# Kernel tuning notes

Hardware: AMD Instinct MI355X
Metric: run time of the kernel (lower is better)

## Reference

```python
import jax, jax.numpy as jnp
import numpy as np

MAX_LOGIT = 30.0
COV_WEIGHT = 1.0


def setup_inputs() -> dict:
    key = jax.random.key(0)
    ks = jax.random.split(key, 8)
    B, T, S, H = 8, 100, 400, 256
    sc = 1.0 / np.sqrt(H)
    return {
        "decoder_outputs": jax.random.normal(ks[0], (B, T, H), jnp.float32),
        "encoder_outputs": jax.random.normal(ks[1], (B, S, H), jnp.float32),
        "src_mask": jnp.zeros((B, S), dtype=bool),
        "W_h": jax.random.normal(ks[2], (H, H), jnp.float32) * sc,
        "W_s": jax.random.normal(ks[3], (H, H), jnp.float32) * sc,
        "w_c": jax.random.normal(ks[4], (H,), jnp.float32) * sc,  # Linear(1,H) weight
        "v": jax.random.normal(ks[5], (H,), jnp.float32) * sc,    # Linear(H,1) weight
        "b_attn": jnp.zeros((H,), jnp.float32),
    }


def reference(decoder_outputs, encoder_outputs, src_mask, W_h, W_s, w_c, v, b_attn):
    B, T, H = decoder_outputs.shape
    S = encoder_outputs.shape[1]
    neg_inf = jnp.float32(-jnp.inf)

    Wh = jnp.einsum('bsh,hk->bsk', encoder_outputs, W_h)   # [B,S,H]
    Ws = jnp.einsum('bth,hk->btk', decoder_outputs, W_s)   # [B,T,H]
    # E_base: [B,T,S,H]
    E_base = Wh[:, None, :, :] + Ws[:, :, None, :] + b_attn

    def logits(x):
        e = jnp.einsum('btsh,h->bts', jnp.tanh(x), v)
        e = jnp.clip(e, -MAX_LOGIT, MAX_LOGIT)
        return jnp.where(src_mask[:, None, :], neg_inf, e)

    A_prelim = jax.nn.softmax(logits(E_base), axis=-1)      # [B,T,S]
    cum = jnp.cumsum(A_prelim, axis=1)
    cov_shifted = jnp.concatenate(
        [jnp.zeros((B, 1, S), A_prelim.dtype), cum[:, :-1, :]], axis=1)  # [B,T,S]

    # W_c applied to scalar coverage: outer product with w_c -> [B,T,S,H]
    E_final = logits(E_base + cov_shifted[..., None] * w_c)
    A_final = jax.nn.softmax(E_final, axis=-1)              # [B,T,S]

    context = jnp.einsum('bts,bsh->bth', A_final, encoder_outputs)
    cov_loss = (COV_WEIGHT * jnp.sum(jnp.minimum(A_final, cov_shifted), axis=-1).mean())[None]
    return context, A_final, cov_loss
```

## Files before the change

kernel.cpp:

```cpp
#include <hip/hip_runtime.h>
#include <math.h>

#define B_ 8
#define T_ 100
#define S_ 400
#define H_ 256
#define HQ_ (H_ / 4)
#define BT_ (B_ * T_)
#define MAXL 30.0f
#define K_EXP 2.885390081777927f

#define AF_OFF (BT_ * H_)
#define LOSS_OFF (BT_ * H_ + BT_ * S_)

#define EWHT_OFF 0
#define EWSB_OFF (B_ * H_ * S_)
#define ACOV_OFF (EWSB_OFF + BT_ * H_)

#define EC1 0.6931471806f
#define EC2 0.2402265070f
#define EC3 0.0555041087f
#define EC4 0.0096181291f

__device__ __forceinline__ float wave_sum(float p) {
#pragma unroll
    for (int off = 32; off; off >>= 1) p += __shfl_xor(p, off, 64);
    return p;
}

__device__ __forceinline__ float wave_max(float p) {
#pragma unroll
    for (int off = 32; off; off >>= 1) p = fmaxf(p, __shfl_xor(p, off, 64));
    return p;
}

#define ROWS 8
__global__ __launch_bounds__(256) void k_gemm(
    const float* __restrict__ dec, const float* __restrict__ enc,
    const float* __restrict__ W_h, const float* __restrict__ W_s,
    const float* __restrict__ b_attn,
    float* __restrict__ EWhT4, float* __restrict__ EWsb) {
    const int tid = threadIdx.x;
    const int blk = blockIdx.x;
    const int NB_ENC = (B_ * S_) / ROWS;

    float acc[ROWS];
#pragma unroll
    for (int r = 0; r < ROWS; ++r) acc[r] = 0.f;

    if (blk < NB_ENC) {
        const int r0 = blk * ROWS;
        const int b = r0 / S_, s0 = r0 - b * S_;
        const float* in = enc + (size_t)r0 * H_;
        const float* Wp = W_h + tid;
#pragma unroll 4
        for (int h = 0; h < H_; ++h) {
            float w = Wp[(size_t)h * H_];
#pragma unroll
            for (int r = 0; r < ROWS; ++r)
                acc[r] = fmaf(in[r * H_ + h], w, acc[r]);
        }
        float* o = EWhT4 + (((size_t)b * HQ_ + (tid >> 2)) * S_ + s0) * 4 + (tid & 3);
#pragma unroll
        for (int r = 0; r < ROWS; ++r)
            o[r * 4] = __builtin_amdgcn_exp2f(K_EXP * acc[r]);
    } else {
        const int bt0 = (blk - NB_ENC) * ROWS;
        const float* in = dec + (size_t)bt0 * H_;
        const float* Wp = W_s + tid;
        const float bias = b_attn[tid];
#pragma unroll 4
        for (int h = 0; h < H_; ++h) {
            float w = Wp[(size_t)h * H_];
#pragma unroll
            for (int r = 0; r < ROWS; ++r)
                acc[r] = fmaf(in[r * H_ + h], w, acc[r]);
        }
#pragma unroll
        for (int r = 0; r < ROWS; ++r)
            EWsb[(size_t)(bt0 + r) * H_ + tid] =
                __builtin_amdgcn_exp2f(K_EXP * (acc[r] + bias));
    }
}

__global__ __launch_bounds__(1024) void k_prelim(
    const float* __restrict__ EWhT4, const float* __restrict__ EWsb,
    const float* __restrict__ v,
    const unsigned char* __restrict__ mask,
    float* __restrict__ A) {
    __shared__ float red[32];
    const int blk = blockIdx.x;
    const int b = blk & 7;
    const int tp = blk >> 3;
    const int tid = threadIdx.x;
    const int hh = tid >> 9;
    const int s = tid & 511;
    const int bt = b * T_ + 2 * tp + hh;
    const int lane = tid & 63;
    const int wid = tid >> 6;
    const bool act = (s < S_);

    const float4 vv4 = *reinterpret_cast<const float4*>(v + 4 * lane);
    const float sumv = wave_sum((vv4.x + vv4.y) + (vv4.z + vv4.w));

    const float* E = EWsb + (size_t)bt * H_;
    float acc = 0.f;
    if (act) {
        const float4* eq = reinterpret_cast<const float4*>(
                               EWhT4 + (size_t)b * HQ_ * S_ * 4) + s;
#pragma unroll 4
        for (int hq = 0; hq < HQ_; ++hq) {
            const float4 Ew = eq[(size_t)hq * S_];
            const int h = 4 * hq;
            const float v0 = v[h], v1 = v[h + 1], v2 = v[h + 2], v3 = v[h + 3];
            float p0 = fmaf(Ew.x, E[h], 1.f);
            float p1 = fmaf(Ew.y, E[h + 1], 1.f);
            float p2 = fmaf(Ew.z, E[h + 2], 1.f);
            float p3 = fmaf(Ew.w, E[h + 3], 1.f);
            float p01 = p0 * p1, p23 = p2 * p3;
            float num = fmaf(fmaf(v0, p1, v1 * p0), p23,
                             fmaf(v2, p3, v3 * p2) * p01);
            acc = fmaf(num, __builtin_amdgcn_rcpf(p01 * p23), acc);
        }
    }

    float e = -INFINITY;
    if (act) {
        e = fminf(fmaxf(sumv - 2.f * acc, -MAXL), MAXL);
        if (mask[(size_t)b * S_ + s]) e = -INFINITY;
    }

    float mx = wave_max(e);
    if (lane == 0) red[wid] = mx;
    __syncthreads();
    {
        const float* r8 = red + 8 * hh;
        mx = fmaxf(fmaxf(fmaxf(r8[0], r8[1]), fmaxf(r8[2], r8[3])),
                   fmaxf(fmaxf(r8[4], r8[5]), fmaxf(r8[6], r8[7])));
    }

    float p = act ? __expf(e - mx) : 0.f;
    float sm = wave_sum(p);
    if (lane == 0) red[16 + wid] = sm;
    __syncthreads();
    {
        const float* r8 = red + 16 + 8 * hh;
        sm = ((r8[0] + r8[1]) + (r8[2] + r8[3])) +
             ((r8[4] + r8[5]) + (r8[6] + r8[7]));
    }

    if (act) A[(size_t)bt * S_ + s] = p * __builtin_amdgcn_rcpf(sm);
}

__global__ __launch_bounds__(64) void k_cumsum(float* __restrict__ A,
                                               float* __restrict__ out) {
    const int idx = blockIdx.x * 64 + threadIdx.x;
    if (idx == 0) out[LOSS_OFF] = 0.f;
    if (idx >= B_ * S_) return;
    const int b = idx / S_;
    const int s = idx - b * S_;
    float* col = A + (size_t)b * T_ * S_ + s;
    float run = 0.f;
#pragma unroll 10
    for (int t = 0; t < T_; ++t) {
        float a = col[(size_t)t * S_];
        col[(size_t)t * S_] = run;
        run += a;
    }
}

__global__ __launch_bounds__(1024) void k_final(
    const float* __restrict__ EWhT4, const float* __restrict__ EWsb,
    const float* __restrict__ v, const float* __restrict__ w_c,
    const float* __restrict__ cov,
    const unsigned char* __restrict__ mask,
    const float* __restrict__ enc,
    float* __restrict__ out) {
    __shared__ float e_lds[2][512];
    __shared__ float ctxp[2 * H_];
    __shared__ float red[32];
    const int blk = blockIdx.x;
    const int b = blk & 7;
    const int tp = blk >> 3;
    const int bt0 = b * T_ + 2 * tp;
    const int tid = threadIdx.x;
    const int hh = tid >> 9;
    const int s = tid & 511;
    const int bt = bt0 + hh;
    const int lane = tid & 63;
    const int wid = tid >> 6;
    const bool act = (s < S_);

    const float4 vv4 = *reinterpret_cast<const float4*>(v + 4 * lane);
    const float sumv = wave_sum((vv4.x + vv4.y) + (vv4.z + vv4.w));

    float c = 0.f;
    if (act) c = cov[(size_t)bt * S_ + s];
    const float ck = K_EXP * c;

    const float* E = EWsb + (size_t)bt * H_;
    float acc = 0.f;
    if (act) {
        const float4* eq = reinterpret_cast<const float4*>(
                               EWhT4 + (size_t)b * HQ_ * S_ * 4) + s;
#pragma unroll 2
        for (int hq = 0; hq < HQ_; ++hq) {
            const float4 Ew = eq[(size_t)hq * S_];
            const int h = 4 * hq;
            const float v0 = v[h], v1 = v[h + 1], v2 = v[h + 2], v3 = v[h + 3];
            float x0 = ck * w_c[h];
            float x1 = ck * w_c[h + 1];
            float x2 = ck * w_c[h + 2];
            float x3 = ck * w_c[h + 3];
            float Ec0 = fmaf(x0, fmaf(x0, fmaf(x0, fmaf(x0, EC4, EC3), EC2), EC1), 1.f);
            float Ec1 = fmaf(x1, fmaf(x1, fmaf(x1, fmaf(x1, EC4, EC3), EC2), EC1), 1.f);
            float Ec2 = fmaf(x2, fmaf(x2, fmaf(x2, fmaf(x2, EC4, EC3), EC2), EC1), 1.f);
            float Ec3 = fmaf(x3, fmaf(x3, fmaf(x3, fmaf(x3, EC4, EC3), EC2), EC1), 1.f);
            float p0 = fmaf(Ew.x * E[h], Ec0, 1.f);
            float p1 = fmaf(Ew.y * E[h + 1], Ec1, 1.f);
            float p2 = fmaf(Ew.z * E[h + 2], Ec2, 1.f);
            float p3 = fmaf(Ew.w * E[h + 3], Ec3, 1.f);
            float p01 = p0 * p1, p23 = p2 * p3;
            float num = fmaf(fmaf(v0, p1, v1 * p0), p23,
                             fmaf(v2, p3, v3 * p2) * p01);
            acc = fmaf(num, __builtin_amdgcn_rcpf(p01 * p23), acc);
        }
    }

    float e = -INFINITY;
    if (act) {
        e = fminf(fmaxf(sumv - 2.f * acc, -MAXL), MAXL);
        if (mask[(size_t)b * S_ + s]) e = -INFINITY;
    }

    float mx = wave_max(e);
    if (lane == 0) red[wid] = mx;
    __syncthreads();
    {
        const float* r8 = red + 8 * hh;
        mx = fmaxf(fmaxf(fmaxf(r8[0], r8[1]), fmaxf(r8[2], r8[3])),
                   fmaxf(fmaxf(r8[4], r8[5]), fmaxf(r8[6], r8[7])));
    }

    float p = act ? __expf(e - mx) : 0.f;
    float sm = wave_sum(p);
    if (lane == 0) red[16 + wid] = sm;
    __syncthreads();
    {
        const float* r8 = red + 16 + 8 * hh;
        sm = ((r8[0] + r8[1]) + (r8[2] + r8[3])) +
             ((r8[4] + r8[5]) + (r8[6] + r8[7]));
    }

    const float a = act ? p * __builtin_amdgcn_rcpf(sm) : 0.f;

    float lp = act ? fminf(a, c) : 0.f;
    lp = wave_sum(lp);
    if (lane == 0) red[wid] = lp;

    if (act) {
        e_lds[hh][s] = a;
        out[AF_OFF + (size_t)bt * S_ + s] = a;
    }
    __syncthreads();

    if (tid == 0) {
        float tot = 0.f;
#pragma unroll
        for (int i = 0; i < 16; ++i) tot += red[i];
        atomicAdd(out + LOSS_OFF, tot * (1.0f / (B_ * T_)));
    }

    const int q = tid >> 8;
    const int h = tid & (H_ - 1);
    const int ts = q & 1;
    const int sb = (q >> 1) * (S_ / 2);
    const float* el = e_lds[ts];
    const float* eb = enc + ((size_t)b * S_ + sb) * H_ + h;
    float q0 = 0.f, q1 = 0.f, q2 = 0.f, q3 = 0.f;
#pragma unroll 5
    for (int j = 0; j < S_ / 2; j += 4) {
        q0 = fmaf(el[sb + j], eb[(size_t)j * H_], q0);
        q1 = fmaf(el[sb + j + 1], eb[(size_t)(j + 1) * H_], q1);
        q2 = fmaf(el[sb + j + 2], eb[(size_t)(j + 2) * H_], q2);
        q3 = fmaf(el[sb + j + 3], eb[(size_t)(j + 3) * H_], q3);
    }
    const float r = (q0 + q1) + (q2 + q3);
    if ((q >> 1) == 0) ctxp[ts * H_ + h] = r;
    __syncthreads();
    if ((q >> 1) == 1)
        out[(size_t)(bt0 + ts) * H_ + h] = ctxp[ts * H_ + h] + r;
}

extern "C" void kernel_launch(void* const* d_in, const int* in_sizes, int n_in,
                              void* d_out, int out_size, void* d_ws, size_t ws_size,
                              hipStream_t stream) {
    const float* dec = (const float*)d_in[0];
    const float* enc = (const float*)d_in[1];
    const unsigned char* mask = (const unsigned char*)d_in[2];
    const float* W_h = (const float*)d_in[3];
    const float* W_s = (const float*)d_in[4];
    const float* w_c = (const float*)d_in[5];
    const float* v = (const float*)d_in[6];
    const float* b_attn = (const float*)d_in[7];

    float* out = (float*)d_out;
    float* ws = (float*)d_ws;
    float* EWhT4 = ws + EWHT_OFF;
    float* EWsb = ws + EWSB_OFF;
    float* Acov = ws + ACOV_OFF;

    const int nb_gemm = (B_ * S_) / ROWS + BT_ / ROWS;
    const int nb_pair = B_ * (T_ / 2);
    k_gemm<<<nb_gemm, 256, 0, stream>>>(dec, enc, W_h, W_s, b_attn, EWhT4, EWsb);
    k_prelim<<<nb_pair, 1024, 0, stream>>>(EWhT4, EWsb, v, mask, Acov);
    k_cumsum<<<(B_ * S_ + 63) / 64, 64, 0, stream>>>(Acov, out);
    k_final<<<nb_pair, 1024, 0, stream>>>(EWhT4, EWsb, v, w_c, Acov, mask, enc, out);
}
```

Measured before the change: 177.2 us.

## Split H across half-blocks so each Ew load serves two decoder rows

```diff
diff --git a/kernel.cpp b/kernel.cpp
--- a/kernel.cpp
+++ b/kernel.cpp
@@ -16,11 +16,6 @@
 #define EWHT_OFF 0
 #define EWSB_OFF (B_ * H_ * S_)
 #define ACOV_OFF (EWSB_OFF + BT_ * H_)
-
-#define EC1 0.6931471806f
-#define EC2 0.2402265070f
-#define EC3 0.0555041087f
-#define EC4 0.0096181291f
 
 __device__ __forceinline__ float wave_sum(float p) {
 #pragma unroll
@@ -88,14 +83,15 @@
     const float* __restrict__ v,
     const unsigned char* __restrict__ mask,
     float* __restrict__ A) {
+    __shared__ float part[2][512][2];
     __shared__ float red[32];
     const int blk = blockIdx.x;
     const int b = blk & 7;
     const int tp = blk >> 3;
+    const int bt0 = b * T_ + 2 * tp;
     const int tid = threadIdx.x;
     const int hh = tid >> 9;
     const int s = tid & 511;
-    const int bt = b * T_ + 2 * tp + hh;
     const int lane = tid & 63;
     const int wid = tid >> 6;
     const bool act = (s < S_);
@@ -103,30 +99,49 @@
     const float4 vv4 = *reinterpret_cast<const float4*>(v + 4 * lane);
     const float sumv = wave_sum((vv4.x + vv4.y) + (vv4.z + vv4.w));
 
-    const float* E = EWsb + (size_t)bt * H_;
-    float acc = 0.f;
+    const float* E0 = EWsb + (size_t)bt0 * H_;
+    const float* E1 = E0 + H_;
+    float acc0 = 0.f, acc1 = 0.f;
     if (act) {
         const float4* eq = reinterpret_cast<const float4*>(
-                               EWhT4 + (size_t)b * HQ_ * S_ * 4) + s;
+                               EWhT4 + (size_t)b * HQ_ * S_ * 4) +
+                           s + (size_t)(hh * 32) * S_;
 #pragma unroll 4
-        for (int hq = 0; hq < HQ_; ++hq) {
+        for (int hq = 0; hq < 32; ++hq) {
             const float4 Ew = eq[(size_t)hq * S_];
-            const int h = 4 * hq;
+            const int h = hh * 128 + 4 * hq;
             const float v0 = v[h], v1 = v[h + 1], v2 = v[h + 2], v3 = v[h + 3];
-            float p0 = fmaf(Ew.x, E[h], 1.f);
-            float p1 = fmaf(Ew.y, E[h + 1], 1.f);
-            float p2 = fmaf(Ew.z, E[h + 2], 1.f);
-            float p3 = fmaf(Ew.w, E[h + 3], 1.f);
-            float p01 = p0 * p1, p23 = p2 * p3;
-            float num = fmaf(fmaf(v0, p1, v1 * p0), p23,
-                             fmaf(v2, p3, v3 * p2) * p01);
-            acc = fmaf(num, __builtin_amdgcn_rcpf(p01 * p23), acc);
+            {
+                float p0 = fmaf(Ew.x, E0[h], 1.f);
+                float p1 = fmaf(Ew.y, E0[h + 1], 1.f);
+                float p2 = fmaf(Ew.z, E0[h + 2], 1.f);
+                float p3 = fmaf(Ew.w, E0[h + 3], 1.f);
+                float p01 = p0 * p1, p23 = p2 * p3;
+                float num = fmaf(fmaf(v0, p1, v1 * p0), p23,
+                                 fmaf(v2, p3, v3 * p2) * p01);
+                acc0 = fmaf(num, __builtin_amdgcn_rcpf(p01 * p23), acc0);
+            }
+            {
+                float p0 = fmaf(Ew.x, E1[h], 1.f);
+                float p1 = fmaf(Ew.y, E1[h + 1], 1.f);
+                float p2 = fmaf(Ew.z, E1[h + 2], 1.f);
+                float p3 = fmaf(Ew.w, E1[h + 3], 1.f);
+                float p01 = p0 * p1, p23 = p2 * p3;
+                float num = fmaf(fmaf(v0, p1, v1 * p0), p23,
+                                 fmaf(v2, p3, v3 * p2) * p01);
+                acc1 = fmaf(num, __builtin_amdgcn_rcpf(p01 * p23), acc1);
+            }
         }
     }
 
+    part[hh][s][0] = acc0;
+    part[hh][s][1] = acc1;
+    __syncthreads();
+
+    const float full = part[0][s][hh] + part[1][s][hh];
     float e = -INFINITY;
     if (act) {
-        e = fminf(fmaxf(sumv - 2.f * acc, -MAXL), MAXL);
+        e = fminf(fmaxf(sumv - 2.f * full, -MAXL), MAXL);
         if (mask[(size_t)b * S_ + s]) e = -INFINITY;
     }
 
@@ -149,7 +164,7 @@
              ((r8[4] + r8[5]) + (r8[6] + r8[7]));
     }
 
-    if (act) A[(size_t)bt * S_ + s] = p * __builtin_amdgcn_rcpf(sm);
+    if (act) A[(size_t)(bt0 + hh) * S_ + s] = p * __builtin_amdgcn_rcpf(sm);
 }
 
 __global__ __launch_bounds__(64) void k_cumsum(float* __restrict__ A,
@@ -176,8 +191,9 @@
     const unsigned char* __restrict__ mask,
     const float* __restrict__ enc,
     float* __restrict__ out) {
+    __shared__ float part[2][512][2];
     __shared__ float e_lds[2][512];
-    __shared__ float ctxp[2 * H_];
+    __shared__ float ctxq[4][H_][2];
     __shared__ float red[32];
     const int blk = blockIdx.x;
     const int b = blk & 7;
@@ -186,7 +202,6 @@
     const int tid = threadIdx.x;
     const int hh = tid >> 9;
     const int s = tid & 511;
-    const int bt = bt0 + hh;
     const int lane = tid & 63;
     const int wid = tid >> 6;
     const bool act = (s < S_);
@@ -194,42 +209,57 @@
     const float4 vv4 = *reinterpret_cast<const float4*>(v + 4 * lane);
     const float sumv = wave_sum((vv4.x + vv4.y) + (vv4.z + vv4.w));
 
-    float c = 0.f;
-    if (act) c = cov[(size_t)bt * S_ + s];
-    const float ck = K_EXP * c;
-
-    const float* E = EWsb + (size_t)bt * H_;
-    float acc = 0.f;
+    float c0 = 0.f, c1 = 0.f;
+    if (act) {
+        c0 = cov[(size_t)bt0 * S_ + s];
+        c1 = cov[(size_t)(bt0 + 1) * S_ + s];
+    }
+    const float ck0 = K_EXP * c0, ck1 = K_EXP * c1;
+
+    const float* E0 = EWsb + (size_t)bt0 * H_;
+    const float* E1 = E0 + H_;
+    float acc0 = 0.f, acc1 = 0.f;
     if (act) {
         const float4* eq = reinterpret_cast<const float4*>(
-                               EWhT4 + (size_t)b * HQ_ * S_ * 4) + s;
+                               EWhT4 + (size_t)b * HQ_ * S_ * 4) +
+                           s + (size_t)(hh * 32) * S_;
 #pragma unroll 2
-        for (int hq = 0; hq < HQ_; ++hq) {
+        for (int hq = 0; hq < 32; ++hq) {
             const float4 Ew = eq[(size_t)hq * S_];
-            const int h = 4 * hq;
+            const int h = hh * 128 + 4 * hq;
             const float v0 = v[h], v1 = v[h + 1], v2 = v[h + 2], v3 = v[h + 3];
-            float x0 = ck * w_c[h];
-            float x1 = ck * w_c[h + 1];
-            float x2 = ck * w_c[h + 2];
-            float x3 = ck * w_c[h + 3];
-            float Ec0 = fmaf(x0, fmaf(x0, fmaf(x0, fmaf(x0, EC4, EC3), EC2), EC1), 1.f);
-            float Ec1 = fmaf(x1, fmaf(x1, fmaf(x1, fmaf(x1, EC4, EC3), EC2), EC1), 1.f);
-            float Ec2 = fmaf(x2, fmaf(x2, fmaf(x2, fmaf(x2, EC4, EC3), EC2), EC1), 1.f);
-            float Ec3 = fmaf(x3, fmaf(x3, fmaf(x3, fmaf(x3, EC4, EC3), EC2), EC1), 1.f);
-            float p0 = fmaf(Ew.x * E[h], Ec0, 1.f);
-            float p1 = fmaf(Ew.y * E[h + 1], Ec1, 1.f);
-            float p2 = fmaf(Ew.z * E[h + 2], Ec2, 1.f);
-            float p3 = fmaf(Ew.w * E[h + 3], Ec3, 1.f);
-            float p01 = p0 * p1, p23 = p2 * p3;
-            float num = fmaf(fmaf(v0, p1, v1 * p0), p23,
-                             fmaf(v2, p3, v3 * p2) * p01);
-            acc = fmaf(num, __builtin_amdgcn_rcpf(p01 * p23), acc);
+            const float w0 = w_c[h], w1 = w_c[h + 1], w2 = w_c[h + 2], w3 = w_c[h + 3];
+            {
+                float p0 = fmaf(Ew.x * E0[h], __builtin_amdgcn_exp2f(ck0 * w0), 1.f);
+                float p1 = fmaf(Ew.y * E0[h + 1], __builtin_amdgcn_exp2f(ck0 * w1), 1.f);
+                float p2 = fmaf(Ew.z * E0[h + 2], __builtin_amdgcn_exp2f(ck0 * w2), 1.f);
+                float p3 = fmaf(Ew.w * E0[h + 3], __builtin_amdgcn_exp2f(ck0 * w3), 1.f);
+                float p01 = p0 * p1, p23 = p2 * p3;
+                float num = fmaf(fmaf(v0, p1, v1 * p0), p23,
+                                 fmaf(v2, p3, v3 * p2) * p01);
+                acc0 = fmaf(num, __builtin_amdgcn_rcpf(p01 * p23), acc0);
+            }
+            {
+                float p0 = fmaf(Ew.x * E1[h], __builtin_amdgcn_exp2f(ck1 * w0), 1.f);
+                float p1 = fmaf(Ew.y * E1[h + 1], __builtin_amdgcn_exp2f(ck1 * w1), 1.f);
+                float p2 = fmaf(Ew.z * E1[h + 2], __builtin_amdgcn_exp2f(ck1 * w2), 1.f);
+                float p3 = fmaf(Ew.w * E1[h + 3], __builtin_amdgcn_exp2f(ck1 * w3), 1.f);
+                float p01 = p0 * p1, p23 = p2 * p3;
+                float num = fmaf(fmaf(v0, p1, v1 * p0), p23,
+                                 fmaf(v2, p3, v3 * p2) * p01);
+                acc1 = fmaf(num, __builtin_amdgcn_rcpf(p01 * p23), acc1);
+            }
         }
     }
 
+    part[hh][s][0] = acc0;
+    part[hh][s][1] = acc1;
+    __syncthreads();
+
+    const float full = part[0][s][hh] + part[1][s][hh];
     float e = -INFINITY;
     if (act) {
-        e = fminf(fmaxf(sumv - 2.f * acc, -MAXL), MAXL);
+        e = fminf(fmaxf(sumv - 2.f * full, -MAXL), MAXL);
         if (mask[(size_t)b * S_ + s]) e = -INFINITY;
     }
 
@@ -253,14 +283,15 @@
     }
 
     const float a = act ? p * __builtin_amdgcn_rcpf(sm) : 0.f;
-
-    float lp = act ? fminf(a, c) : 0.f;
+    const float c_own = hh ? c1 : c0;
+
+    float lp = act ? fminf(a, c_own) : 0.f;
     lp = wave_sum(lp);
     if (lane == 0) red[wid] = lp;
 
     if (act) {
         e_lds[hh][s] = a;
-        out[AF_OFF + (size_t)bt * S_ + s] = a;
+        out[AF_OFF + (size_t)(bt0 + hh) * S_ + s] = a;
     }
     __syncthreads();
 
@@ -273,23 +304,23 @@
 
     const int q = tid >> 8;
     const int h = tid & (H_ - 1);
-    const int ts = q & 1;
-    const int sb = (q >> 1) * (S_ / 2);
-    const float* el = e_lds[ts];
+    const int sb = q * (S_ / 4);
     const float* eb = enc + ((size_t)b * S_ + sb) * H_ + h;
-    float q0 = 0.f, q1 = 0.f, q2 = 0.f, q3 = 0.f;
-#pragma unroll 5
-    for (int j = 0; j < S_ / 2; j += 4) {
-        q0 = fmaf(el[sb + j], eb[(size_t)j * H_], q0);
-        q1 = fmaf(el[sb + j + 1], eb[(size_t)(j + 1) * H_], q1);
-        q2 = fmaf(el[sb + j + 2], eb[(size_t)(j + 2) * H_], q2);
-        q3 = fmaf(el[sb + j + 3], eb[(size_t)(j + 3) * H_], q3);
-    }
-    const float r = (q0 + q1) + (q2 + q3);
-    if ((q >> 1) == 0) ctxp[ts * H_ + h] = r;
-    __syncthreads();
-    if ((q >> 1) == 1)
-        out[(size_t)(bt0 + ts) * H_ + h] = ctxp[ts * H_ + h] + r;
+    float r0 = 0.f, r1 = 0.f;
+#pragma unroll 4
+    for (int j = 0; j < S_ / 4; ++j) {
+        const float w = eb[(size_t)j * H_];
+        r0 = fmaf(e_lds[0][sb + j], w, r0);
+        r1 = fmaf(e_lds[1][sb + j], w, r1);
+    }
+    ctxq[q][h][0] = r0;
+    ctxq[q][h][1] = r1;
+    __syncthreads();
+    if (q < 2) {
+        const float tot = ((ctxq[0][h][q] + ctxq[1][h][q]) +
+                           (ctxq[2][h][q] + ctxq[3][h][q]));
+        out[(size_t)(bt0 + q) * H_ + h] = tot;
+    }
 }
 
 extern "C" void kernel_launch(void* const* d_in, const int* in_sizes, int n_in,
```

Result: slower. 183.0 us (+3.3%).
